# Performance work log

Hardware: AMD Instinct MI355X
Metric: run time of the kernel (lower is better)

The kernel has to match this reference:

```python
import jax, jax.numpy as jnp
import numpy as np

B, DAYS, N, E = 2, 8, 10000, 80000
C_IN, C_OUT, H = 32, 32, 4
NEG_SLOPE = 0.2


def setup_inputs() -> dict:
    key = jax.random.key(0)
    ks = jax.random.split(key, 7)
    x = jax.random.randint(ks[0], (B, DAYS, N), 0, N)
    adjacency = jax.random.randint(ks[1], (2, E), 0, N)
    embedding = jax.random.normal(ks[2], (N, C_IN), dtype=jnp.float32)
    # GATConv linear: in_channels -> heads*out_channels
    W = jax.random.normal(ks[3], (C_IN, H * C_OUT), dtype=jnp.float32) / np.sqrt(C_IN)
    att_src = jax.random.normal(ks[4], (H, C_OUT), dtype=jnp.float32) / np.sqrt(C_OUT)
    att_dst = jax.random.normal(ks[5], (H, C_OUT), dtype=jnp.float32) / np.sqrt(C_OUT)
    bias = jnp.zeros((H * C_OUT,), dtype=jnp.float32)
    return {"x": x, "adjacency": adjacency, "embedding": embedding,
            "W": W, "att_src": att_src, "att_dst": att_dst, "bias": bias}


def _gat_forward(feat, src, dst, W, att_src, att_dst, bias):
    # feat: [G, N, C_IN]; same edge list shared across the G graphs
    G = feat.shape[0]
    xh = (feat @ W).reshape(G, N, H, C_OUT)              # [G,N,H,C]
    a_src = jnp.einsum('gnhc,hc->gnh', xh, att_src)       # [G,N,H]
    a_dst = jnp.einsum('gnhc,hc->gnh', xh, att_dst)
    alpha = a_src[:, src] + a_dst[:, dst]                 # [G,Et,H]
    alpha = jnp.where(alpha >= 0, alpha, NEG_SLOPE * alpha)

    def per_graph(al, msgs):
        # segment softmax over incoming edges of each dst node
        m = jax.ops.segment_max(al, dst, num_segments=N)  # [N,H]
        e = jnp.exp(al - m[dst])                          # [Et,H]
        s = jax.ops.segment_sum(e, dst, num_segments=N)
        w = e / (s[dst] + 1e-16)
        out = jax.ops.segment_sum(w[..., None] * msgs, dst, num_segments=N)
        return out                                        # [N,H,C]

    out = jax.vmap(per_graph)(alpha, xh[:, src])          # [G,N,H,C]
    return out.reshape(G, N, H * C_OUT) + bias


def reference(x, adjacency, embedding, W, att_src, att_dst, bias):
    Bd, Dd = x.shape[0], x.shape[1]
    feat = embedding[x].reshape(-1, N, C_IN)              # [G,N,C_IN]
    # GATConv default add_self_loops=True
    loops = jnp.arange(N, dtype=adjacency.dtype)
    src = jnp.concatenate([adjacency[0], loops])
    dst = jnp.concatenate([adjacency[1], loops])
    out = _gat_forward(feat, src, dst, W, att_src, att_dst, bias)
    return out.reshape(Bd, Dd, -1)
```

## Files before the change

### kernel.cpp

```cpp
#include <hip/hip_runtime.h>
#include <hip/hip_bf16.h>
#include <math.h>

#define C_IN 32
#define H 4
#define C_OUT 32
#define HC (H * C_OUT)
#define NEG_SLOPE 0.2f
#define CSR_STRIDE 64

typedef float v2f __attribute__((ext_vector_type(2)));

#define RPB 16
__global__ __launch_bounds__(256) void build_kernel(
        const int* __restrict__ adj, int E, int N,
        int* __restrict__ deg, int* __restrict__ csr,
        const float* __restrict__ emb, const float* __restrict__ W,
        const float* __restrict__ att_src, const float* __restrict__ att_dst,
        __hip_bfloat16* __restrict__ T, float* __restrict__ ta_src,
        float* __restrict__ ta_dst, int tblocks) {
    if ((int)blockIdx.x >= tblocks) {
        int e = (blockIdx.x - tblocks) * 256 + threadIdx.x;
        int Et = E + N;
        if (e < Et) {
            int s = (e < E) ? adj[e] : (e - E);
            int d = (e < E) ? adj[E + e] : (e - E);
            int pos = atomicAdd(&deg[d], 1);
            if (pos < CSR_STRIDE) csr[(d << 6) + pos] = s;
        }
        return;
    }
    int t = threadIdx.x;
    int sub = t >> 7;
    int tc = t & 127;
    int h = tc >> 5, c = tc & 31;
    int base = blockIdx.x * RPB;
    int nmax = (N - base < RPB) ? (N - base) : RPB;

    float wcol[C_IN];
#pragma unroll
    for (int k = 0; k < C_IN; k++) wcol[k] = W[k * HC + tc];
    float as = att_src[h * C_OUT + c];
    float adw = att_dst[h * C_OUT + c];

    for (int it = sub; it < nmax; it += 2) {
        int r = __builtin_amdgcn_readfirstlane(base + it);
        const float* ep = emb + (size_t)r * C_IN;
        float acc = 0.f;
#pragma unroll
        for (int k = 0; k < C_IN; k++) acc += ep[k] * wcol[k];
        T[(size_t)r * HC + tc] = __float2bfloat16(acc);
        float ps = acc * as, pd = acc * adw;
#pragma unroll
        for (int o = 16; o; o >>= 1) {
            ps += __shfl_xor(ps, o, 32);
            pd += __shfl_xor(pd, o, 32);
        }
        if (c == 0) {
            ta_src[r * H + h] = ps;
            ta_dst[r * H + h] = pd;
        }
    }
}

__global__ __launch_bounds__(256) void agg_kernel(
        const int* __restrict__ deg, const int* __restrict__ csr,
        const int* __restrict__ x, const unsigned int* __restrict__ Tu,
        const float* __restrict__ ta_src, const float* __restrict__ ta_dst,
        const float* __restrict__ bias, float* __restrict__ out, int N, int G) {
    __shared__ float w_lds[CSR_STRIDE][16][4];
    __shared__ int   xs8_lds[16][65];
    __shared__ float ds_lds[16][4];

    int t = threadIdx.x;

    int gA = t >> 4;
    int e0 = t & 15;
    int es = (t >> 2) & 3;
    int hB = t & 3;
    int wid = t >> 6;
    int lane = t & 63;
    int lg = lane >> 4;
    int li = lane & 15;
    int gj = wid * 4 + lg;
    int hh = li >> 2;
    unsigned int li16 = (unsigned int)(li << 4);
    const float4* bp = (const float4*)(bias + li * 8);
    float4 b0 = bp[0], b1 = bp[1];

    for (int n = blockIdx.x; n < N; n += gridDim.x) {
        int dg = deg[n];
        if (dg > CSR_STRIDE) dg = CSR_STRIDE;
        int dgp4 = (dg + 3) & ~3;
        const int* cb = csr + (n << 6);

        {
            const int* xg = x + (size_t)gA * N;
            for (int c0 = 0; c0 < dg; c0 += 16) {
                int slot = c0 + e0;
                int sv = cb[slot];
                int s = (slot < dg) ? sv : 0;
                xs8_lds[gA][slot] = xg[s] << 8;
            }
        }
        __syncthreads();

        {
            int xgn = x[(size_t)gA * N + n];
            float adv = ta_dst[xgn * H + hB];
            float dpart = 0.f;
            for (int c0 = 0; c0 < dgp4; c0 += 4) {
                int slot = c0 + es;
                int xs = xs8_lds[gA][slot] >> 8;
                float a = ta_src[xs * H + hB] + adv;
                a = fmaxf(a, NEG_SLOPE * a);
                float w = (slot < dg) ? __expf(a) : 0.f;
                w_lds[slot][gA][hB] = w;
                dpart += w;
            }
            dpart += __shfl_xor(dpart, 4, 64);
            dpart += __shfl_xor(dpart, 8, 64);
            if (es == 0) ds_lds[gA][hB] = dpart;
        }
        __syncthreads();

        v2f a0 = {0.f, 0.f}, a1 = {0.f, 0.f}, a2 = {0.f, 0.f}, a3 = {0.f, 0.f};

#pragma unroll 4
        for (int e = 0; e < dgp4; e++) {
            unsigned int off = (unsigned int)xs8_lds[gj][e] + li16;
            float w = w_lds[e][gj][hh];
            v2f w2 = {w, w};
            uint4 u = *(const uint4*)((const char*)Tu + off);
            v2f t0 = {__uint_as_float(u.x << 16),
                      __uint_as_float(u.x & 0xffff0000u)};
            v2f t1 = {__uint_as_float(u.y << 16),
                      __uint_as_float(u.y & 0xffff0000u)};
            v2f t2 = {__uint_as_float(u.z << 16),
                      __uint_as_float(u.z & 0xffff0000u)};
            v2f t3 = {__uint_as_float(u.w << 16),
                      __uint_as_float(u.w & 0xffff0000u)};
            a0 += w2 * t0;
            a1 += w2 * t1;
            a2 += w2 * t2;
            a3 += w2 * t3;
        }

        float inv = __builtin_amdgcn_rcpf(ds_lds[gj][hh] + 1e-16f);
        float4 o0 = {a0.x * inv + b0.x, a0.y * inv + b0.y,
                     a1.x * inv + b0.z, a1.y * inv + b0.w};
        float4 o1 = {a2.x * inv + b1.x, a2.y * inv + b1.y,
                     a3.x * inv + b1.z, a3.y * inv + b1.w};
        float* op = out + (size_t)gj * N * HC + (size_t)n * HC + li * 8;
        *(float4*)op = o0;
        *(float4*)(op + 4) = o1;

        __syncthreads();
    }
}

extern "C" void kernel_launch(void* const* d_in, const int* in_sizes, int n_in,
                              void* d_out, int out_size, void* d_ws, size_t ws_size,
                              hipStream_t stream) {
    const int*   x       = (const int*)d_in[0];
    const int*   adj     = (const int*)d_in[1];
    const float* emb     = (const float*)d_in[2];
    const float* W       = (const float*)d_in[3];
    const float* att_src = (const float*)d_in[4];
    const float* att_dst = (const float*)d_in[5];
    const float* bias    = (const float*)d_in[6];
    float* out = (float*)d_out;

    const int N  = in_sizes[2] / C_IN;
    const int GN = in_sizes[0];
    const int G  = GN / N;
    const int E  = in_sizes[1] / 2;
    const int Et = E + N;

    char* ws = (char*)d_ws;
    size_t o = 0;
    auto carve = [&](size_t bytes) -> void* {
        void* p = ws + o;
        o = (o + bytes + 255) & ~(size_t)255;
        return p;
    };
    __hip_bfloat16* T = (__hip_bfloat16*)carve((size_t)N * HC * sizeof(__hip_bfloat16));
    float* ta_src  = (float*)carve((size_t)N * H * sizeof(float));
    float* ta_dst  = (float*)carve((size_t)N * H * sizeof(float));
    int*   deg     = (int*)carve((size_t)N * sizeof(int));
    int*   csr     = (int*)carve((size_t)N * CSR_STRIDE * sizeof(int));

    hipMemsetAsync(deg, 0, (size_t)N * sizeof(int), stream);

    int tblocks = (N + RPB - 1) / RPB;
    int fblocks = (Et + 255) / 256;
    build_kernel<<<tblocks + fblocks, 256, 0, stream>>>(
        adj, E, N, deg, csr, emb, W, att_src, att_dst, T, ta_src, ta_dst, tblocks);

    int ablocks = (N + 3) / 4;
    agg_kernel<<<ablocks, 256, 0, stream>>>(deg, csr, x,
                                            (const unsigned int*)T, ta_src, ta_dst,
                                            bias, out, N, G);
}
```

Measured before the change: 152.5 us.

## Fuse attention weight computation into aggregation loop and launch one block per node

```diff
diff --git a/kernel.cpp b/kernel.cpp
--- a/kernel.cpp
+++ b/kernel.cpp
@@ -68,16 +68,28 @@
         const int* __restrict__ x, const unsigned int* __restrict__ Tu,
         const float* __restrict__ ta_src, const float* __restrict__ ta_dst,
         const float* __restrict__ bias, float* __restrict__ out, int N, int G) {
-    __shared__ float w_lds[CSR_STRIDE][16][4];
-    __shared__ int   xs8_lds[16][65];
-    __shared__ float ds_lds[16][4];
+    __shared__ int xs8_lds[16][69];
 
     int t = threadIdx.x;
+    int n = blockIdx.x;
+    int dg = deg[n];
+    if (dg > CSR_STRIDE) dg = CSR_STRIDE;
+    int dgp4 = (dg + 3) & ~3;
+    const int* cb = csr + (n << 6);
 
-    int gA = t >> 4;
-    int e0 = t & 15;
-    int es = (t >> 2) & 3;
-    int hB = t & 3;
+    {
+        int gA = t >> 4;
+        int e0 = t & 15;
+        const int* xg = x + (size_t)gA * N;
+        for (int c0 = 0; c0 < dg; c0 += 16) {
+            int slot = c0 + e0;
+            int sv = cb[slot];
+            int s = (slot < dg) ? sv : 0;
+            xs8_lds[gA][slot] = xg[s] << 8;
+        }
+    }
+    __syncthreads();
+
     int wid = t >> 6;
     int lane = t & 63;
     int lg = lane >> 4;
@@ -85,78 +97,43 @@
     int gj = wid * 4 + lg;
     int hh = li >> 2;
     unsigned int li16 = (unsigned int)(li << 4);
+
+    int xgn = x[(size_t)gj * N + n];
+    float ad = ta_dst[xgn * H + hh];
+
+    v2f a0 = {0.f, 0.f}, a1 = {0.f, 0.f}, a2 = {0.f, 0.f}, a3 = {0.f, 0.f};
+    float dsum = 0.f;
+
+#pragma unroll 4
+    for (int e = 0; e < dgp4; e++) {
+        int xs8 = xs8_lds[gj][e];
+        int xs = xs8 >> 8;
+        float a = ta_src[xs * H + hh] + ad;
+        a = fmaxf(a, NEG_SLOPE * a);
+        float w = (e < dg) ? __expf(a) : 0.f;
+        uint4 u = *(const uint4*)((const char*)Tu + (unsigned int)xs8 + li16);
+        v2f w2 = {w, w};
+        v2f t0 = {__uint_as_float(u.x << 16), __uint_as_float(u.x & 0xffff0000u)};
+        v2f t1 = {__uint_as_float(u.y << 16), __uint_as_float(u.y & 0xffff0000u)};
+        v2f t2 = {__uint_as_float(u.z << 16), __uint_as_float(u.z & 0xffff0000u)};
+        v2f t3 = {__uint_as_float(u.w << 16), __uint_as_float(u.w & 0xffff0000u)};
+        a0 += w2 * t0;
+        a1 += w2 * t1;
+        a2 += w2 * t2;
+        a3 += w2 * t3;
+        dsum += w;
+    }
+
+    float inv = __builtin_amdgcn_rcpf(dsum + 1e-16f);
     const float4* bp = (const float4*)(bias + li * 8);
     float4 b0 = bp[0], b1 = bp[1];
-
-    for (int n = blockIdx.x; n < N; n += gridDim.x) {
-        int dg = deg[n];
-        if (dg > CSR_STRIDE) dg = CSR_STRIDE;
-        int dgp4 = (dg + 3) & ~3;
-        const int* cb = csr + (n << 6);
-
-        {
-            const int* xg = x + (size_t)gA * N;
-            for (int c0 = 0; c0 < dg; c0 += 16) {
-                int slot = c0 + e0;
-                int sv = cb[slot];
-                int s = (slot < dg) ? sv : 0;
-                xs8_lds[gA][slot] = xg[s] << 8;
-            }
-        }
-        __syncthreads();
-
-        {
-            int xgn = x[(size_t)gA * N + n];
-            float adv = ta_dst[xgn * H + hB];
-            float dpart = 0.f;
-            for (int c0 = 0; c0 < dgp4; c0 += 4) {
-                int slot = c0 + es;
-                int xs = xs8_lds[gA][slot] >> 8;
-                float a = ta_src[xs * H + hB] + adv;
-                a = fmaxf(a, NEG_SLOPE * a);
-                float w = (slot < dg) ? __expf(a) : 0.f;
-                w_lds[slot][gA][hB] = w;
-                dpart += w;
-            }
-            dpart += __shfl_xor(dpart, 4, 64);
-            dpart += __shfl_xor(dpart, 8, 64);
-            if (es == 0) ds_lds[gA][hB] = dpart;
-        }
-        __syncthreads();
-
-        v2f a0 = {0.f, 0.f}, a1 = {0.f, 0.f}, a2 = {0.f, 0.f}, a3 = {0.f, 0.f};
-
-#pragma unroll 4
-        for (int e = 0; e < dgp4; e++) {
-            unsigned int off = (unsigned int)xs8_lds[gj][e] + li16;
-            float w = w_lds[e][gj][hh];
-            v2f w2 = {w, w};
-            uint4 u = *(const uint4*)((const char*)Tu + off);
-            v2f t0 = {__uint_as_float(u.x << 16),
-                      __uint_as_float(u.x & 0xffff0000u)};
-            v2f t1 = {__uint_as_float(u.y << 16),
-                      __uint_as_float(u.y & 0xffff0000u)};
-            v2f t2 = {__uint_as_float(u.z << 16),
-                      __uint_as_float(u.z & 0xffff0000u)};
-            v2f t3 = {__uint_as_float(u.w << 16),
-                      __uint_as_float(u.w & 0xffff0000u)};
-            a0 += w2 * t0;
-            a1 += w2 * t1;
-            a2 += w2 * t2;
-            a3 += w2 * t3;
-        }
-
-        float inv = __builtin_amdgcn_rcpf(ds_lds[gj][hh] + 1e-16f);
-        float4 o0 = {a0.x * inv + b0.x, a0.y * inv + b0.y,
-                     a1.x * inv + b0.z, a1.y * inv + b0.w};
-        float4 o1 = {a2.x * inv + b1.x, a2.y * inv + b1.y,
-                     a3.x * inv + b1.z, a3.y * inv + b1.w};
-        float* op = out + (size_t)gj * N * HC + (size_t)n * HC + li * 8;
-        *(float4*)op = o0;
-        *(float4*)(op + 4) = o1;
-
-        __syncthreads();
-    }
+    float4 o0 = {a0.x * inv + b0.x, a0.y * inv + b0.y,
+                 a1.x * inv + b0.z, a1.y * inv + b0.w};
+    float4 o1 = {a2.x * inv + b1.x, a2.y * inv + b1.y,
+                 a3.x * inv + b1.z, a3.y * inv + b1.w};
+    float* op = out + (size_t)gj * N * HC + (size_t)n * HC + li * 8;
+    *(float4*)op = o0;
+    *(float4*)(op + 4) = o1;
 }
 
 extern "C" void kernel_launch(void* const* d_in, const int* in_sizes, int n_in,
@@ -197,8 +174,7 @@
     build_kernel<<<tblocks + fblocks, 256, 0, stream>>>(
         adj, E, N, deg, csr, emb, W, att_src, att_dst, T, ta_src, ta_dst, tblocks);
 
-    int ablocks = (N + 3) / 4;
-    agg_kernel<<<ablocks, 256, 0, stream>>>(deg, csr, x,
-                                            (const unsigned int*)T, ta_src, ta_dst,
-                                            bias, out, N, G);
+    agg_kernel<<<N, 256, 0, stream>>>(deg, csr, x,
+                                      (const unsigned int*)T, ta_src, ta_dst,
+                                      bias, out, N, G);
 }
```

Measured after the change: 147.6 us, median of 2. 3.2% less time.
